# Performance work log

Measured on AMD Instinct MI355X. Metric: run time of the kernel, lower is better.

The kernel has to match this reference:

```python
import jax, jax.numpy as jnp
import numpy as np

B, S, H = 512, 100, 768
LAMB = 0.8

def setup_inputs() -> dict:
    key = jax.random.key(0)
    k1, k2, k3, k4 = jax.random.split(key, 4)
    scale = 1.0 / np.sqrt(H)
    return {
        "sent_vec": jax.random.normal(k1, (B, S, H), dtype=jnp.float32),
        "mask_cls": jnp.ones((B, S), dtype=jnp.int32),
        "W_cont": jax.random.normal(k2, (1, H), dtype=jnp.float32) * scale,
        "W_sim": jax.random.normal(k3, (H, H), dtype=jnp.float32) * scale,
        "W_rel": jax.random.normal(k4, (H, H), dtype=jnp.float32) * scale,
        "b_matrix": jnp.zeros((1, 1), dtype=jnp.float32),
    }

def reference(sent_vec, mask_cls, W_cont, W_sim, W_rel, b_matrix):
    # sent_vec: [B,S,H], mask_cls: [B,S] (all ones -> true_dim == S)
    m = mask_cls.astype(sent_vec.dtype)                       # [B,S]
    mask2 = m[:, :, None] * m[:, None, :]                     # mask_my_own [B,S,S]

    # Score_Cont[b,i,j] = W_cont . sent_vec[b,i]
    cont = jnp.einsum('h,bih->bi', W_cont[0], sent_vec)       # [B,S]
    # Score_Sim[b,i,j] = sent_i W_sim sent_j^T, masked
    sim = jnp.einsum('bih,hk,bjk->bij', sent_vec, W_sim, sent_vec) * mask2
    # Score_rel[b,i,j] = sent_i W_rel d_rep, masked
    d_rep = sent_vec.mean(axis=1)                             # [B,H]
    rel = jnp.einsum('bih,hk,bk->bi', sent_vec, W_rel, d_rep) # [B,S]

    q = jax.nn.sigmoid(rel[:, :, None] * mask2 + cont[:, :, None] + sim + b_matrix[0, 0])
    q = q * mask2                                             # [B,S,S]

    # D = diag(column sums of q); q @ D^{-1} divides columns by sum_vec
    sum_vec = q.sum(axis=1)                                   # [B,S]
    qD = q / sum_vec[:, None, :]                              # [B,S,S]

    I = jnp.eye(S, dtype=q.dtype)
    M = I[None, :, :] - LAMB * qD                             # [B,S,S]
    y = jnp.full((B, S, 1), 1.0 / S, dtype=q.dtype)
    # Final_score = (1-lamb) * inv(I - lamb q D^-1) @ y  (solve == inverse@mm)
    score = (1.0 - LAMB) * jnp.linalg.solve(M, y)[:, :, 0]    # [B,S]
    return score
```

## Files before the change

kernel.cpp:

```cpp
#include <hip/hip_runtime.h>
#include <math.h>

#define BB 512
#define SS 100
#define HH 768

typedef __bf16 bf16x8 __attribute__((ext_vector_type(8)));
typedef __bf16 bf16x4 __attribute__((ext_vector_type(4)));
typedef float f32x4 __attribute__((ext_vector_type(4)));
typedef float f32x16 __attribute__((ext_vector_type(16)));

__device__ __forceinline__ void gld16(const void* g, void* l) {
    __builtin_amdgcn_global_load_lds((const __attribute__((address_space(1))) char*)g,
                                     (__attribute__((address_space(3))) char*)l, 16, 0, 0);
}

__global__ __launch_bounds__(256) void k_drep(const float* __restrict__ X,
                                              float* __restrict__ drep) {
    int b = blockIdx.x, g = blockIdx.y;
    int lane = threadIdx.x & 63, w = threadIdx.x >> 6;
    const float4* xb = (const float4*)(X + (size_t)b * SS * HH);
    int c4 = g * 64 + lane;
    float4 s = {0.f, 0.f, 0.f, 0.f};
    for (int r = w; r < SS; r += 4) {
        float4 v = xb[r * 192 + c4];
        s.x += v.x; s.y += v.y; s.z += v.z; s.w += v.w;
    }
    __shared__ float4 red[4][64];
    red[w][lane] = s;
    __syncthreads();
    if (w == 0) {
        float4 a0 = red[0][lane], a1 = red[1][lane], a2 = red[2][lane], a3 = red[3][lane];
        float4 o;
        o.x = (a0.x + a1.x + a2.x + a3.x) * (1.0f / SS);
        o.y = (a0.y + a1.y + a2.y + a3.y) * (1.0f / SS);
        o.z = (a0.z + a1.z + a2.z + a3.z) * (1.0f / SS);
        o.w = (a0.w + a1.w + a2.w + a3.w) * (1.0f / SS);
        ((float4*)(drep + (size_t)b * HH))[c4] = o;
    }
}

__global__ __launch_bounds__(256) void k_gemm_nt(const float* __restrict__ A,
                                                 const float* __restrict__ Bm,
                                                 float* __restrict__ C,
                                                 int N, int K) {
    __shared__ float As[64 * 20];
    __shared__ float Bs[64 * 20];
    int tid = threadIdx.x;
    int ty = tid >> 4, tx = tid & 15;
    int m0 = blockIdx.y * 64, n0 = blockIdx.x * 64;
    int lr = tid >> 2, lc = (tid & 3) * 4;
    float acc[4][4] = {};
    for (int kt = 0; kt < K; kt += 16) {
        *(float4*)(As + lr * 20 + lc) = *(const float4*)(A + (size_t)(m0 + lr) * K + kt + lc);
        *(float4*)(Bs + lr * 20 + lc) = *(const float4*)(Bm + (size_t)(n0 + lr) * K + kt + lc);
        __syncthreads();
        #pragma unroll
        for (int k = 0; k < 16; k += 2) {
            float2 ar[4], br[4];
            #pragma unroll
            for (int ii = 0; ii < 4; ++ii) ar[ii] = *(const float2*)(As + (ty + 16 * ii) * 20 + k);
            #pragma unroll
            for (int jj = 0; jj < 4; ++jj) br[jj] = *(const float2*)(Bs + (tx + 16 * jj) * 20 + k);
            #pragma unroll
            for (int ii = 0; ii < 4; ++ii)
                #pragma unroll
                for (int jj = 0; jj < 4; ++jj)
                    acc[ii][jj] = fmaf(ar[ii].y, br[jj].y, fmaf(ar[ii].x, br[jj].x, acc[ii][jj]));
        }
        __syncthreads();
    }
    #pragma unroll
    for (int ii = 0; ii < 4; ++ii)
        #pragma unroll
        for (int jj = 0; jj < 4; ++jj)
            C[(size_t)(m0 + ty + 16 * ii) * N + n0 + tx + 16 * jj] = acc[ii][jj];
}

__global__ __launch_bounds__(256) void k_splitw(const float* __restrict__ W,
                                                __bf16* __restrict__ th,
                                                __bf16* __restrict__ tl) {
    __shared__ float tile[32][33];
    int bn = blockIdx.x * 32, bk = blockIdx.y * 32;
    int tx = threadIdx.x & 31, ty = threadIdx.x >> 5;
    for (int r = ty; r < 32; r += 8)
        tile[r][tx] = W[(size_t)(bk + r) * HH + bn + tx];
    __syncthreads();
    for (int r = ty; r < 32; r += 8) {
        float v = tile[tx][r];
        __bf16 hv = (__bf16)v;
        size_t idx = (size_t)(bn + r) * HH + bk + tx;
        th[idx] = hv;
        tl[idx] = (__bf16)(v - (float)hv);
    }
}

__global__ __launch_bounds__(512) void k_split_contrel(const float* __restrict__ X,
                                                       const float* __restrict__ Wc,
                                                       const float* __restrict__ tmat,
                                                       const float* __restrict__ bmat,
                                                       __bf16* __restrict__ Xh,
                                                       __bf16* __restrict__ Xl,
                                                       float* __restrict__ avec,
                                                       int b_off) {
    __shared__ float4 u4[192];
    int lb = blockIdx.x, half = blockIdx.y;
    int b = b_off + lb;
    int tid = threadIdx.x, lane = tid & 63, w = tid >> 6;
    for (int c = tid; c < 192; c += 512) {
        float4 wc = ((const float4*)Wc)[c];
        float4 tm = ((const float4*)(tmat + (size_t)b * HH))[c];
        float4 o = {wc.x + tm.x, wc.y + tm.y, wc.z + tm.z, wc.w + tm.w};
        u4[c] = o;
    }
    __syncthreads();
    float b00 = bmat[0];
    const float4* xb = (const float4*)(X + (size_t)b * SS * HH);
    bf16x4* xh4 = (bf16x4*)(Xh + (size_t)lb * SS * HH);
    bf16x4* xl4 = (bf16x4*)(Xl + (size_t)lb * SS * HH);
    int rend = half * 50 + 50;
    for (int r = half * 50 + w; r < rend; r += 8) {
        float s = 0.f;
        #pragma unroll
        for (int cc = 0; cc < 3; ++cc) {
            int c = cc * 64 + lane;
            float4 v = xb[r * 192 + c];
            float4 uu = u4[c];
            s = fmaf(v.x, uu.x, fmaf(v.y, uu.y, fmaf(v.z, uu.z, fmaf(v.w, uu.w, s))));
            bf16x4 hv, lv;
            hv[0] = (__bf16)v.x; lv[0] = (__bf16)(v.x - (float)hv[0]);
            hv[1] = (__bf16)v.y; lv[1] = (__bf16)(v.y - (float)hv[1]);
            hv[2] = (__bf16)v.z; lv[2] = (__bf16)(v.z - (float)hv[2]);
            hv[3] = (__bf16)v.w; lv[3] = (__bf16)(v.w - (float)hv[3]);
            xh4[r * 192 + c] = hv;
            xl4[r * 192 + c] = lv;
        }
        #pragma unroll
        for (int off = 32; off > 0; off >>= 1) s += __shfl_down(s, off);
        if (lane == 0) avec[(size_t)b * SS + r] = s + b00;
    }
}

__global__ __launch_bounds__(512) void k_gemm1_mfma(const __bf16* __restrict__ Ah_g,
                                                    const __bf16* __restrict__ Al_g,
                                                    const __bf16* __restrict__ Bh_g,
                                                    const __bf16* __restrict__ Bl_g,
                                                    __bf16* __restrict__ Yh,
                                                    __bf16* __restrict__ Yl) {
    __shared__ __align__(16) __bf16 lds[2 * 32768];
    const int tid = threadIdx.x;
    const int wave = tid >> 6, lane = tid & 63;
    const int wy = wave >> 2, wx = wave & 3;
    const int nwg = gridDim.x;
    const int lid = blockIdx.x;
    const int q8 = nwg >> 3, r8 = nwg & 7;
    const int xcd = lid & 7, idx = lid >> 3;
    const int tile = (xcd < r8 ? xcd * (q8 + 1) : r8 * (q8 + 1) + (xcd - r8) * q8) + idx;
    const size_t m0 = (size_t)(tile / 3) * 256;
    const int n0 = (tile % 3) * 256;

    const int srow = tid >> 2;
    const int scol = ((lane & 3) ^ ((lane >> 3) & 3)) * 8;
    const int wbase = wave * 512;

    const int arow = wy * 128 + (lane & 31);
    const int brow = wx * 64 + (lane & 31);
    const int sw = (lane >> 1) & 3;

    f32x16 acc[4][2] = {};

    auto stage = [&](int buf, int kt) {
        __bf16* base = lds + buf * 32768;
        const size_t ga0 = (m0 + srow) * HH + kt + scol;
        const size_t ga1 = ga0 + (size_t)128 * HH;
        const size_t gb0 = (size_t)(n0 + srow) * HH + kt + scol;
        const size_t gb1 = gb0 + (size_t)128 * HH;
        gld16(Ah_g + ga0, base + wbase);
        gld16(Ah_g + ga1, base + 4096 + wbase);
        gld16(Al_g + ga0, base + 8192 + wbase);
        gld16(Al_g + ga1, base + 12288 + wbase);
        gld16(Bh_g + gb0, base + 16384 + wbase);
        gld16(Bh_g + gb1, base + 20480 + wbase);
        gld16(Bl_g + gb0, base + 24576 + wbase);
        gld16(Bl_g + gb1, base + 28672 + wbase);
    };
    auto compute = [&](int buf) {
        const __bf16* Ah_s = lds + buf * 32768;
        const __bf16* Al_s = Ah_s + 8192;
        const __bf16* Bh_s = Ah_s + 16384;
        const __bf16* Bl_s = Ah_s + 24576;
        #pragma unroll
        for (int kh = 0; kh < 2; ++kh) {
            const int ko = (((kh << 1) + (lane >> 5)) ^ sw) << 3;
            bf16x8 fah[4], fal[4], fbh[2], fbl[2];
            #pragma unroll
            for (int t = 0; t < 4; ++t) {
                fah[t] = *(const bf16x8*)(Ah_s + (arow + t * 32) * 32 + ko);
                fal[t] = *(const bf16x8*)(Al_s + (arow + t * 32) * 32 + ko);
            }
            #pragma unroll
            for (int t = 0; t < 2; ++t) {
                fbh[t] = *(const bf16x8*)(Bh_s + (brow + t * 32) * 32 + ko);
                fbl[t] = *(const bf16x8*)(Bl_s + (brow + t * 32) * 32 + ko);
            }
            #pragma unroll
            for (int ti = 0; ti < 4; ++ti)
                #pragma unroll
                for (int tj = 0; tj < 2; ++tj) {
                    acc[ti][tj] = __builtin_amdgcn_mfma_f32_32x32x16_bf16(fal[ti], fbh[tj], acc[ti][tj], 0, 0, 0);
                    acc[ti][tj] = __builtin_amdgcn_mfma_f32_32x32x16_bf16(fah[ti], fbl[tj], acc[ti][tj], 0, 0, 0);
                    acc[ti][tj] = __builtin_amdgcn_mfma_f32_32x32x16_bf16(fah[ti], fbh[tj], acc[ti][tj], 0, 0, 0);
                }
        }
    };

    stage(0, 0);
    int cur = 0;
    for (int kt = 32; kt < HH; kt += 32) {
        stage(cur ^ 1, kt);
        asm volatile("s_waitcnt vmcnt(8)" ::: "memory");
        __builtin_amdgcn_s_barrier();
        compute(cur);
        __builtin_amdgcn_s_barrier();
        cur ^= 1;
    }
    asm volatile("s_waitcnt vmcnt(0)" ::: "memory");
    __builtin_amdgcn_s_barrier();
    compute(cur);

    const int rbase = 4 * (lane >> 5);
    const int colb = lane & 31;
    #pragma unroll
    for (int ti = 0; ti < 4; ++ti) {
        #pragma unroll
        for (int tj = 0; tj < 2; ++tj) {
            int col = n0 + wx * 64 + tj * 32 + colb;
            #pragma unroll
            for (int r = 0; r < 16; ++r) {
                int row = wy * 128 + ti * 32 + (r & 3) + 8 * (r >> 2) + rbase;
                float v = acc[ti][tj][r];
                __bf16 hv = (__bf16)v;
                size_t idx = (m0 + row) * HH + col;
                Yh[idx] = hv;
                Yl[idx] = (__bf16)(v - (float)hv);
            }
        }
    }
}

__global__ __launch_bounds__(256) void k_gemm2_mfma(const __bf16* __restrict__ Yh,
                                                    const __bf16* __restrict__ Yl,
                                                    const __bf16* __restrict__ Xh,
                                                    const __bf16* __restrict__ Xl,
                                                    const float* __restrict__ avec,
                                                    float* __restrict__ q, int b_off) {
    __shared__ __align__(16) __bf16 lds[2 * 4 * 4096];
    __shared__ float av_s[SS];
    const int bl = blockIdx.x;
    const int b = b_off + bl;
    const __bf16* Ah_g = Yh + (size_t)bl * SS * HH;
    const __bf16* Al_g = Yl + (size_t)bl * SS * HH;
    const __bf16* Bh_g = Xh + (size_t)bl * SS * HH;
    const __bf16* Bl_g = Xl + (size_t)bl * SS * HH;
    const int tid = threadIdx.x;
    const int wave = tid >> 6, lane = tid & 63;
    const int wy = wave >> 1, wx = wave & 1;
    if (tid < SS) av_s[tid] = avec[(size_t)b * SS + tid];

    const int srow_raw = wave * 32 + (lane >> 2);
    const int scol = ((lane & 3) ^ ((lane >> 3) & 3)) * 8;
    const int lds_base = wave * 1024;
    const int r0 = srow_raw < SS ? srow_raw : SS - 1;
    const int r1 = (srow_raw + 16) < SS ? (srow_raw + 16) : SS - 1;

    const int arow = wy * 64 + (lane & 31);
    const int brow = wx * 64 + (lane & 31);
    const int sw = (lane >> 1) & 3;

    f32x16 acc[2][2] = {};

    auto stage = [&](int buf, int kt) {
        __bf16* base = lds + buf * 16384;
        const size_t ga0 = (size_t)r0 * HH + kt + scol;
        const size_t ga1 = (size_t)r1 * HH + kt + scol;
        gld16(Ah_g + ga0, base + lds_base);
        gld16(Ah_g + ga1, base + lds_base + 512);
        gld16(Al_g + ga0, base + 4096 + lds_base);
        gld16(Al_g + ga1, base + 4096 + lds_base + 512);
        gld16(Bh_g + ga0, base + 8192 + lds_base);
        gld16(Bh_g + ga1, base + 8192 + lds_base + 512);
        gld16(Bl_g + ga0, base + 12288 + lds_base);
        gld16(Bl_g + ga1, base + 12288 + lds_base + 512);
    };
    auto compute = [&](int buf) {
        const __bf16* As_h = lds + buf * 16384;
        const __bf16* As_l = As_h + 4096;
        const __bf16* Bs_h = As_h + 8192;
        const __bf16* Bs_l = As_h + 12288;
        #pragma unroll
        for (int kh = 0; kh < 2; ++kh) {
            const int ko = (((kh << 1) + (lane >> 5)) ^ sw) << 3;
            bf16x8 fah[2], fal[2], fbh[2], fbl[2];
            #pragma unroll
            for (int t = 0; t < 2; ++t) {
                fah[t] = *(const bf16x8*)(As_h + (arow + t * 32) * 32 + ko);
                fal[t] = *(const bf16x8*)(As_l + (arow + t * 32) * 32 + ko);
                fbh[t] = *(const bf16x8*)(Bs_h + (brow + t * 32) * 32 + ko);
                fbl[t] = *(const bf16x8*)(Bs_l + (brow + t * 32) * 32 + ko);
            }
            #pragma unroll
            for (int ti = 0; ti < 2; ++ti)
                #pragma unroll
                for (int tj = 0; tj < 2; ++tj) {
                    acc[ti][tj] = __builtin_amdgcn_mfma_f32_32x32x16_bf16(fal[ti], fbh[tj], acc[ti][tj], 0, 0, 0);
                    acc[ti][tj] = __builtin_amdgcn_mfma_f32_32x32x16_bf16(fah[ti], fbl[tj], acc[ti][tj], 0, 0, 0);
                    acc[ti][tj] = __builtin_amdgcn_mfma_f32_32x32x16_bf16(fah[ti], fbh[tj], acc[ti][tj], 0, 0, 0);
                }
        }
    };

    stage(0, 0);
    int cur = 0;
    for (int kt = 32; kt < HH; kt += 32) {
        stage(cur ^ 1, kt);
        asm volatile("s_waitcnt vmcnt(8)" ::: "memory");
        __builtin_amdgcn_s_barrier();
        compute(cur);
        __builtin_amdgcn_s_barrier();
        cur ^= 1;
    }
    asm volatile("s_waitcnt vmcnt(0)" ::: "memory");
    __builtin_amdgcn_s_barrier();
    compute(cur);

    float* qb = q + (size_t)b * SS * SS;
    const int rbase = 4 * (lane >> 5);
    const int colb = lane & 31;
    #pragma unroll
    for (int ti = 0; ti < 2; ++ti) {
        #pragma unroll
        for (int tj = 0; tj < 2; ++tj) {
            int j = wx * 64 + tj * 32 + colb;
            if (j >= SS) continue;
            #pragma unroll
            for (int r = 0; r < 16; ++r) {
                int i = wy * 64 + ti * 32 + (r & 3) + 8 * (r >> 2) + rbase;
                if (i >= SS) continue;
                float v = acc[ti][tj][r] + av_s[i];
                qb[(size_t)i * SS + j] = 1.0f / (1.0f + __expf(-v));
            }
        }
    }
}

__global__ __launch_bounds__(128) void k_solve(const float* __restrict__ q,
                                               float* __restrict__ out) {
    __shared__ __align__(16) float m[SS * SS];
    __shared__ __align__(16) float csinv[SS];
    __shared__ __align__(16) float x0[SS], x1[SS];
    int b = blockIdx.x, tid = threadIdx.x;
    const float* qb = q + (size_t)b * SS * SS;
    for (int e4 = tid; e4 < SS * SS / 4; e4 += 128)
        *(float4*)(m + e4 * 4) = *(const float4*)(qb + (size_t)e4 * 4);
    __syncthreads();
    if (tid < SS) {
        float s = 0.f;
        for (int i = 0; i < SS; ++i) s += m[i * SS + tid];
        csinv[tid] = 0.8f / s;
        x0[tid] = 1.0f / SS;
    }
    __syncthreads();
    float4 mreg[25];
    if (tid < SS) {
        #pragma unroll
        for (int j4 = 0; j4 < 25; ++j4) {
            float4 mv = *(const float4*)(m + tid * SS + j4 * 4);
            float4 cv = *(const float4*)(csinv + j4 * 4);
            mreg[j4].x = mv.x * cv.x;
            mreg[j4].y = mv.y * cv.y;
            mreg[j4].z = mv.z * cv.z;
            mreg[j4].w = mv.w * cv.w;
        }
    } else {
        #pragma unroll
        for (int j4 = 0; j4 < 25; ++j4) mreg[j4] = float4{0, 0, 0, 0};
    }
    __syncthreads();
    #pragma unroll 1
    for (int it = 0; it < 56; ++it) {
        const float* xr = (it & 1) ? x1 : x0;
        float* xw = (it & 1) ? x0 : x1;
        if (tid < SS) {
            float sx = 0.f, sy = 0.f, sz = 0.f, sw = 0.f;
            #pragma unroll
            for (int j4 = 0; j4 < 25; ++j4) {
                float4 xv = *(const float4*)(xr + j4 * 4);
                sx = fmaf(mreg[j4].x, xv.x, sx);
                sy = fmaf(mreg[j4].y, xv.y, sy);
                sz = fmaf(mreg[j4].z, xv.z, sz);
                sw = fmaf(mreg[j4].w, xv.w, sw);
            }
            xw[tid] = 0.002f + ((sx + sy) + (sz + sw));
        }
        __syncthreads();
    }
    if (tid < SS) out[(size_t)b * SS + tid] = x0[tid];
}

extern "C" void kernel_launch(void* const* d_in, const int* in_sizes, int n_in,
                              void* d_out, int out_size, void* d_ws, size_t ws_size,
                              hipStream_t stream) {
    (void)in_sizes; (void)n_in; (void)out_size;
    const float* X    = (const float*)d_in[0];
    const float* Wc   = (const float*)d_in[2];
    const float* Wsim = (const float*)d_in[3];
    const float* Wrel = (const float*)d_in[4];
    const float* bmat = (const float*)d_in[5];
    float* out = (float*)d_out;

    char* ws = (char*)d_ws;
    size_t off = 0;
    float*  qbuf = (float*)(ws + off);  off += (size_t)BB * SS * SS * 4;
    float*  drep = (float*)(ws + off);  off += (size_t)BB * HH * 4;
    float*  tmat = (float*)(ws + off);  off += (size_t)BB * HH * 4;
    float*  avec = (float*)(ws + off);  off += (size_t)BB * SS * 4;
    __bf16* Wth  = (__bf16*)(ws + off); off += (size_t)HH * HH * 2;
    __bf16* Wtl  = (__bf16*)(ws + off); off += (size_t)HH * HH * 2;

    int CB = 512;
    while (CB > 128 && off + 4 * (size_t)CB * SS * HH * 2 > ws_size) CB >>= 1;
    size_t xsz = (size_t)CB * SS * HH * 2;
    __bf16* Xh = (__bf16*)(ws + off); off += xsz;
    __bf16* Xl = (__bf16*)(ws + off); off += xsz;
    __bf16* Yh = (__bf16*)(ws + off); off += xsz;
    __bf16* Yl = (__bf16*)(ws + off); off += xsz;

    k_drep<<<dim3(BB, 3), 256, 0, stream>>>(X, drep);
    k_gemm_nt<<<dim3(HH / 64, BB / 64), 256, 0, stream>>>(drep, Wrel, tmat, HH, HH);
    k_splitw<<<dim3(HH / 32, HH / 32), 256, 0, stream>>>(Wsim, Wth, Wtl);

    for (int c = 0; c < BB; c += CB) {
        k_split_contrel<<<dim3(CB, 2), 512, 0, stream>>>(X + (size_t)c * SS * HH, Wc, tmat, bmat, Xh, Xl, avec, c);
        int nblk1 = (CB * SS / 256) * (HH / 256);
        k_gemm1_mfma<<<nblk1, 512, 0, stream>>>(Xh, Xl, Wth, Wtl, Yh, Yl);
        k_gemm2_mfma<<<CB, 256, 0, stream>>>(Yh, Yl, Xh, Xl, avec, qbuf, c);
    }
    k_solve<<<BB, 128, 0, stream>>>(qbuf, out);
}
```

Measured before the change: 709.6 us.

## Interleave global-to-LDS prefetch with MFMA phases in both split-bf16 GEMM kernels

Both MFMA GEMM kernels now issue the next K-tile's global_load_lds in pieces spread across the compute phases instead of in one burst before the barrier. Each kernel waits on a finer vmcnt, and the MFMA blocks are wrapped in s_setprio. The first GEMM also splits its A-fragment loads into halves so fewer registers are live per phase. The aim is to overlap memory traffic with matrix math and smooth out VMEM issue, at the cost of more barriers per iteration and more delicate wait-count correctness.

```diff
diff --git a/kernel.cpp b/kernel.cpp
--- a/kernel.cpp
+++ b/kernel.cpp
@@ -154,8 +154,8 @@
     const int nwg = gridDim.x;
     const int lid = blockIdx.x;
     const int q8 = nwg >> 3, r8 = nwg & 7;
-    const int xcd = lid & 7, idx = lid >> 3;
-    const int tile = (xcd < r8 ? xcd * (q8 + 1) : r8 * (q8 + 1) + (xcd - r8) * q8) + idx;
+    const int xcd = lid & 7, sidx = lid >> 3;
+    const int tile = (xcd < r8 ? xcd * (q8 + 1) : r8 * (q8 + 1) + (xcd - r8) * q8) + sidx;
     const size_t m0 = (size_t)(tile / 3) * 256;
     const int n0 = (tile % 3) * 256;
 
@@ -169,64 +169,97 @@
 
     f32x16 acc[4][2] = {};
 
-    auto stage = [&](int buf, int kt) {
+    auto stage_pair = [&](int buf, int kt, int p) {
         __bf16* base = lds + buf * 32768;
-        const size_t ga0 = (m0 + srow) * HH + kt + scol;
-        const size_t ga1 = ga0 + (size_t)128 * HH;
-        const size_t gb0 = (size_t)(n0 + srow) * HH + kt + scol;
-        const size_t gb1 = gb0 + (size_t)128 * HH;
-        gld16(Ah_g + ga0, base + wbase);
-        gld16(Ah_g + ga1, base + 4096 + wbase);
-        gld16(Al_g + ga0, base + 8192 + wbase);
-        gld16(Al_g + ga1, base + 12288 + wbase);
-        gld16(Bh_g + gb0, base + 16384 + wbase);
-        gld16(Bh_g + gb1, base + 20480 + wbase);
-        gld16(Bl_g + gb0, base + 24576 + wbase);
-        gld16(Bl_g + gb1, base + 28672 + wbase);
+        if (p == 0) {
+            const size_t ga0 = (m0 + srow) * HH + kt + scol;
+            gld16(Ah_g + ga0, base + wbase);
+            gld16(Ah_g + ga0 + (size_t)128 * HH, base + 4096 + wbase);
+        } else if (p == 1) {
+            const size_t ga0 = (m0 + srow) * HH + kt + scol;
+            gld16(Al_g + ga0, base + 8192 + wbase);
+            gld16(Al_g + ga0 + (size_t)128 * HH, base + 12288 + wbase);
+        } else if (p == 2) {
+            const size_t gb0 = (size_t)(n0 + srow) * HH + kt + scol;
+            gld16(Bh_g + gb0, base + 16384 + wbase);
+            gld16(Bh_g + gb0 + (size_t)128 * HH, base + 20480 + wbase);
+        } else {
+            const size_t gb0 = (size_t)(n0 + srow) * HH + kt + scol;
+            gld16(Bl_g + gb0, base + 24576 + wbase);
+            gld16(Bl_g + gb0 + (size_t)128 * HH, base + 28672 + wbase);
+        }
     };
-    auto compute = [&](int buf) {
-        const __bf16* Ah_s = lds + buf * 32768;
+
+    #pragma unroll
+    for (int p = 0; p < 4; ++p) stage_pair(0, 0, p);
+
+    int cur = 0;
+    for (int t = 0; t < HH / 32; ++t) {
+        const int nkt = (t + 1) * 32;
+        const bool pf = nkt < HH;
+        const __bf16* Ah_s = lds + cur * 32768;
         const __bf16* Al_s = Ah_s + 8192;
         const __bf16* Bh_s = Ah_s + 16384;
         const __bf16* Bl_s = Ah_s + 24576;
         #pragma unroll
         for (int kh = 0; kh < 2; ++kh) {
             const int ko = (((kh << 1) + (lane >> 5)) ^ sw) << 3;
-            bf16x8 fah[4], fal[4], fbh[2], fbl[2];
-            #pragma unroll
-            for (int t = 0; t < 4; ++t) {
-                fah[t] = *(const bf16x8*)(Ah_s + (arow + t * 32) * 32 + ko);
-                fal[t] = *(const bf16x8*)(Al_s + (arow + t * 32) * 32 + ko);
+            bf16x8 fbh[2], fbl[2];
+            #pragma unroll
+            for (int half = 0; half < 2; ++half) {
+                const int ph = kh * 2 + half;
+                bf16x8 fah2[2], fal2[2];
+                if (ph == 0) {
+                    if (pf) {
+                        stage_pair(cur ^ 1, nkt, 0);
+                        asm volatile("s_waitcnt vmcnt(2)" ::: "memory");
+                    } else {
+                        asm volatile("s_waitcnt vmcnt(0)" ::: "memory");
+                    }
+                    __builtin_amdgcn_s_barrier();
+                    #pragma unroll
+                    for (int t2 = 0; t2 < 2; ++t2) {
+                        fbh[t2] = *(const bf16x8*)(Bh_s + (brow + t2 * 32) * 32 + ko);
+                        fbl[t2] = *(const bf16x8*)(Bl_s + (brow + t2 * 32) * 32 + ko);
+                        fah2[t2] = *(const bf16x8*)(Ah_s + (arow + t2 * 32) * 32 + ko);
+                        fal2[t2] = *(const bf16x8*)(Al_s + (arow + t2 * 32) * 32 + ko);
+                    }
+                } else {
+                    if (half == 0) {
+                        #pragma unroll
+                        for (int t2 = 0; t2 < 2; ++t2) {
+                            fbh[t2] = *(const bf16x8*)(Bh_s + (brow + t2 * 32) * 32 + ko);
+                            fbl[t2] = *(const bf16x8*)(Bl_s + (brow + t2 * 32) * 32 + ko);
+                            fah2[t2] = *(const bf16x8*)(Ah_s + (arow + t2 * 32) * 32 + ko);
+                            fal2[t2] = *(const bf16x8*)(Al_s + (arow + t2 * 32) * 32 + ko);
+                        }
+                    } else {
+                        #pragma unroll
+                        for (int t2 = 0; t2 < 2; ++t2) {
+                            fah2[t2] = *(const bf16x8*)(Ah_s + (arow + (2 + t2) * 32) * 32 + ko);
+                            fal2[t2] = *(const bf16x8*)(Al_s + (arow + (2 + t2) * 32) * 32 + ko);
+                        }
+                    }
+                    if (pf) stage_pair(cur ^ 1, nkt, ph);
+                    __builtin_amdgcn_s_barrier();
+                }
+                __builtin_amdgcn_s_setprio(1);
+                #pragma unroll
+                for (int tl = 0; tl < 2; ++tl) {
+                    const int ti = half * 2 + tl;
+                    #pragma unroll
+                    for (int tj = 0; tj < 2; ++tj) {
+                        acc[ti][tj] = __builtin_amdgcn_mfma_f32_32x32x16_bf16(fal2[tl], fbh[tj], acc[ti][tj], 0, 0, 0);
+                        acc[ti][tj] = __builtin_amdgcn_mfma_f32_32x32x16_bf16(fah2[tl], fbl[tj], acc[ti][tj], 0, 0, 0);
+                        acc[ti][tj] = __builtin_amdgcn_mfma_f32_32x32x16_bf16(fah2[tl], fbh[tj], acc[ti][tj], 0, 0, 0);
+                    }
+                }
+                __builtin_amdgcn_s_setprio(0);
+                __builtin_amdgcn_s_barrier();
             }
-            #pragma unroll
-            for (int t = 0; t < 2; ++t) {
-                fbh[t] = *(const bf16x8*)(Bh_s + (brow + t * 32) * 32 + ko);
-                fbl[t] = *(const bf16x8*)(Bl_s + (brow + t * 32) * 32 + ko);
-            }
-            #pragma unroll
-            for (int ti = 0; ti < 4; ++ti)
-                #pragma unroll
-                for (int tj = 0; tj < 2; ++tj) {
-                    acc[ti][tj] = __builtin_amdgcn_mfma_f32_32x32x16_bf16(fal[ti], fbh[tj], acc[ti][tj], 0, 0, 0);
-                    acc[ti][tj] = __builtin_amdgcn_mfma_f32_32x32x16_bf16(fah[ti], fbl[tj], acc[ti][tj], 0, 0, 0);
-                    acc[ti][tj] = __builtin_amdgcn_mfma_f32_32x32x16_bf16(fah[ti], fbh[tj], acc[ti][tj], 0, 0, 0);
-                }
-        }
-    };
-
-    stage(0, 0);
-    int cur = 0;
-    for (int kt = 32; kt < HH; kt += 32) {
-        stage(cur ^ 1, kt);
-        asm volatile("s_waitcnt vmcnt(8)" ::: "memory");
-        __builtin_amdgcn_s_barrier();
-        compute(cur);
-        __builtin_amdgcn_s_barrier();
+        }
         cur ^= 1;
     }
-    asm volatile("s_waitcnt vmcnt(0)" ::: "memory");
-    __builtin_amdgcn_s_barrier();
-    compute(cur);
 
     const int rbase = 4 * (lane >> 5);
     const int colb = lane & 31;
@@ -279,7 +312,7 @@
 
     f32x16 acc[2][2] = {};
 
-    auto stage = [&](int buf, int kt) {
+    auto stageA = [&](int buf, int kt) {
         __bf16* base = lds + buf * 16384;
         const size_t ga0 = (size_t)r0 * HH + kt + scol;
         const size_t ga1 = (size_t)r1 * HH + kt + scol;
@@ -287,51 +320,60 @@
         gld16(Ah_g + ga1, base + lds_base + 512);
         gld16(Al_g + ga0, base + 4096 + lds_base);
         gld16(Al_g + ga1, base + 4096 + lds_base + 512);
+    };
+    auto stageB = [&](int buf, int kt) {
+        __bf16* base = lds + buf * 16384;
+        const size_t ga0 = (size_t)r0 * HH + kt + scol;
+        const size_t ga1 = (size_t)r1 * HH + kt + scol;
         gld16(Bh_g + ga0, base + 8192 + lds_base);
         gld16(Bh_g + ga1, base + 8192 + lds_base + 512);
         gld16(Bl_g + ga0, base + 12288 + lds_base);
         gld16(Bl_g + ga1, base + 12288 + lds_base + 512);
     };
-    auto compute = [&](int buf) {
+    auto compute_kh = [&](int buf, int kh) {
         const __bf16* As_h = lds + buf * 16384;
         const __bf16* As_l = As_h + 4096;
         const __bf16* Bs_h = As_h + 8192;
         const __bf16* Bs_l = As_h + 12288;
-        #pragma unroll
-        for (int kh = 0; kh < 2; ++kh) {
-            const int ko = (((kh << 1) + (lane >> 5)) ^ sw) << 3;
-            bf16x8 fah[2], fal[2], fbh[2], fbl[2];
-            #pragma unroll
-            for (int t = 0; t < 2; ++t) {
-                fah[t] = *(const bf16x8*)(As_h + (arow + t * 32) * 32 + ko);
-                fal[t] = *(const bf16x8*)(As_l + (arow + t * 32) * 32 + ko);
-                fbh[t] = *(const bf16x8*)(Bs_h + (brow + t * 32) * 32 + ko);
-                fbl[t] = *(const bf16x8*)(Bs_l + (brow + t * 32) * 32 + ko);
+        const int ko = (((kh << 1) + (lane >> 5)) ^ sw) << 3;
+        bf16x8 fah[2], fal[2], fbh[2], fbl[2];
+        #pragma unroll
+        for (int t = 0; t < 2; ++t) {
+            fah[t] = *(const bf16x8*)(As_h + (arow + t * 32) * 32 + ko);
+            fal[t] = *(const bf16x8*)(As_l + (arow + t * 32) * 32 + ko);
+            fbh[t] = *(const bf16x8*)(Bs_h + (brow + t * 32) * 32 + ko);
+            fbl[t] = *(const bf16x8*)(Bs_l + (brow + t * 32) * 32 + ko);
+        }
+        __builtin_amdgcn_s_setprio(1);
+        #pragma unroll
+        for (int ti = 0; ti < 2; ++ti)
+            #pragma unroll
+            for (int tj = 0; tj < 2; ++tj) {
+                acc[ti][tj] = __builtin_amdgcn_mfma_f32_32x32x16_bf16(fal[ti], fbh[tj], acc[ti][tj], 0, 0, 0);
+                acc[ti][tj] = __builtin_amdgcn_mfma_f32_32x32x16_bf16(fah[ti], fbl[tj], acc[ti][tj], 0, 0, 0);
+                acc[ti][tj] = __builtin_amdgcn_mfma_f32_32x32x16_bf16(fah[ti], fbh[tj], acc[ti][tj], 0, 0, 0);
             }
-            #pragma unroll
-            for (int ti = 0; ti < 2; ++ti)
-                #pragma unroll
-                for (int tj = 0; tj < 2; ++tj) {
-                    acc[ti][tj] = __builtin_amdgcn_mfma_f32_32x32x16_bf16(fal[ti], fbh[tj], acc[ti][tj], 0, 0, 0);
-                    acc[ti][tj] = __builtin_amdgcn_mfma_f32_32x32x16_bf16(fah[ti], fbl[tj], acc[ti][tj], 0, 0, 0);
-                    acc[ti][tj] = __builtin_amdgcn_mfma_f32_32x32x16_bf16(fah[ti], fbh[tj], acc[ti][tj], 0, 0, 0);
-                }
-        }
+        __builtin_amdgcn_s_setprio(0);
     };
 
-    stage(0, 0);
+    stageA(0, 0);
+    stageB(0, 0);
     int cur = 0;
-    for (int kt = 32; kt < HH; kt += 32) {
-        stage(cur ^ 1, kt);
-        asm volatile("s_waitcnt vmcnt(8)" ::: "memory");
+    for (int i = 0; i < HH / 32; ++i) {
+        const int nkt = (i + 1) * 32;
+        if (nkt < HH) {
+            stageA(cur ^ 1, nkt);
+            asm volatile("s_waitcnt vmcnt(4)" ::: "memory");
+        } else {
+            asm volatile("s_waitcnt vmcnt(0)" ::: "memory");
+        }
         __builtin_amdgcn_s_barrier();
-        compute(cur);
+        compute_kh(cur, 0);
+        if (nkt < HH) stageB(cur ^ 1, nkt);
+        compute_kh(cur, 1);
         __builtin_amdgcn_s_barrier();
         cur ^= 1;
     }
-    asm volatile("s_waitcnt vmcnt(0)" ::: "memory");
-    __builtin_amdgcn_s_barrier();
-    compute(cur);
 
     float* qb = q + (size_t)b * SS * SS;
     const int rbase = 4 * (lane >> 5);
```

Measured after the change: 705.0 us. About the same (-0.7%).
